# Performance work log

Measured on AMD Instinct MI355X. Metric: run time of the kernel, lower is better.

The kernel has to match this reference:

```python
import jax, jax.numpy as jnp
import numpy as np

N_NODES = 50000
IN_CH = 128
OUT_CH = 64
N_EDGES = 800000


def setup_inputs() -> dict:
    key = jax.random.key(0)
    k1, k2, k3, k4 = jax.random.split(key, 4)
    z = jax.random.normal(k1, (N_NODES, IN_CH), dtype=jnp.float32)
    edge_index = jax.random.randint(k2, (2, N_EDGES), 0, N_NODES, dtype=jnp.int64)
    # GCNConv params: weight [in, out] (glorot-ish), bias [out]
    W = jax.random.normal(k3, (IN_CH, OUT_CH), dtype=jnp.float32) / np.sqrt(IN_CH)
    b = jnp.zeros((OUT_CH,), dtype=jnp.float32)
    return {"z": z, "edge_index": edge_index, "W": W, "b": b}


def reference(z, edge_index, W, b):
    N = z.shape[0]
    # linear transform first (out_channels < in_channels reduces message traffic)
    x = z @ W  # [N, out]
    # add self-loops
    loop = jnp.arange(N, dtype=edge_index.dtype)
    src = jnp.concatenate([edge_index[0], loop])
    dst = jnp.concatenate([edge_index[1], loop])
    # symmetric normalization deg^-1/2 (degree counted on dst, incl. self-loops)
    deg = jnp.zeros((N,), dtype=x.dtype).at[dst].add(1.0)
    dinv = jnp.where(deg > 0, jax.lax.rsqrt(deg), 0.0)
    norm = dinv[src] * dinv[dst]  # [E+N]
    msg = x[src] * norm[:, None]  # gather + scale
    out = jax.ops.segment_sum(msg, dst, num_segments=N)  # scatter-add
    return jax.nn.relu(out + b)
```

## Files before the change

### kernel.cpp

```cpp
#include <hip/hip_runtime.h>

#define IN_CH 128
#define OUT_CH 64

#define CSHIFT 6
#define BNODES 64
#define NCMAX 1024
#define CAP 1536
#define BIN_EPT 8

typedef __attribute__((ext_vector_type(8))) short bf16x8;
typedef __attribute__((ext_vector_type(4))) float f32x4;

__device__ inline unsigned short f2bf(float x) {
    unsigned int u = __builtin_bit_cast(unsigned int, x);
    return (unsigned short)((u + 0x7FFFu + ((u >> 16) & 1u)) >> 16);
}
__device__ inline float bf2f(unsigned short h) {
    unsigned int u = ((unsigned int)h) << 16;
    return __builtin_bit_cast(float, u);
}

__global__ void bin_edges(const int* __restrict__ ei, int* __restrict__ gctr,
                          unsigned int* __restrict__ ebuf, int E, int NC) {
    __shared__ int cnt[NCMAX];
    __shared__ int gbase[NCMAX];
    for (int i = threadIdx.x; i < NC; i += blockDim.x) cnt[i] = 0;
    __syncthreads();

    unsigned int pk[BIN_EPT];
    int bk[BIN_EPT];
    int e0 = blockIdx.x * (blockDim.x * BIN_EPT) + threadIdx.x;
#pragma unroll
    for (int k = 0; k < BIN_EPT; ++k) {
        int e = e0 + k * blockDim.x;
        if (e < E) {
            int s = ei[e];
            int d = ei[E + e];
            pk[k] = ((unsigned int)d << 16) | (unsigned int)s;
            bk[k] = d >> CSHIFT;
            atomicAdd(&cnt[bk[k]], 1);
        } else bk[k] = -1;
    }
    __syncthreads();
    for (int i = threadIdx.x; i < NC; i += blockDim.x) {
        int c = cnt[i];
        gbase[i] = c ? atomicAdd(&gctr[i], c) : 0;
    }
    __syncthreads();
    for (int i = threadIdx.x; i < NC; i += blockDim.x) cnt[i] = 0;
    __syncthreads();
#pragma unroll
    for (int k = 0; k < BIN_EPT; ++k) {
        if (bk[k] >= 0) {
            int o = gbase[bk[k]] + atomicAdd(&cnt[bk[k]], 1);
            if (o < CAP)
                ebuf[(size_t)bk[k] * CAP + o] = pk[k];
        }
    }
}

__global__ void degree_dinv(const unsigned int* __restrict__ ebuf,
                            const int* __restrict__ gctr,
                            float* __restrict__ dinv, int N) {
    __shared__ int cnt[BNODES];
    const int b = blockIdx.x;
    const int n0 = b << CSHIFT;
    if (threadIdx.x < BNODES) cnt[threadIdx.x] = 0;
    __syncthreads();
    const int ecnt = min(gctr[b], CAP);
    const unsigned int* eb = ebuf + (size_t)b * CAP;
    for (int i = threadIdx.x; i < ecnt; i += blockDim.x)
        atomicAdd(&cnt[(int)(eb[i] >> 16) - n0], 1);
    __syncthreads();
    const int node = n0 + threadIdx.x;
    if (threadIdx.x < BNODES && node < N)
        dinv[node] = rsqrtf((float)(cnt[threadIdx.x] + 1));
}

__global__ void wfrag_prep(const float* __restrict__ W, unsigned short* __restrict__ wf) {
    for (int i = threadIdx.x; i < 4 * 4 * 64 * 8; i += blockDim.x) {
        int j    = i & 7;
        int lane = (i >> 3) & 63;
        int kk   = (i >> 9) & 3;
        int nt   = i >> 11;
        int k = kk * 32 + ((lane >> 4) & 3) * 8 + j;
        int n = nt * 16 + (lane & 15);
        wf[i] = f2bf(W[k * OUT_CH + n]);
    }
}

__global__ void gemm_mfma(const float* __restrict__ z,
                          const unsigned short* __restrict__ wfrag,
                          const float* __restrict__ dinv,
                          unsigned short* __restrict__ y, int N) {
    const int lane = threadIdx.x & 63;
    const int wid  = threadIdx.x >> 6;
    const int row0 = blockIdx.x * 64 + wid * 16;

    bf16x8 bfr[4][4];
#pragma unroll
    for (int nt = 0; nt < 4; ++nt)
#pragma unroll
        for (int kk = 0; kk < 4; ++kk)
            bfr[nt][kk] = *(const bf16x8*)&wfrag[(((nt * 4 + kk) * 64) + lane) * 8];

    f32x4 acc[4];
#pragma unroll
    for (int nt = 0; nt < 4; ++nt) acc[nt] = (f32x4){0.f, 0.f, 0.f, 0.f};

    const int arow = row0 + (lane & 15);
    const int zrow = (arow < N) ? arow : (N - 1);
    const int sub  = lane >> 4;
    const float* zr = z + (size_t)zrow * IN_CH + sub * 8;

#pragma unroll
    for (int kk = 0; kk < 4; ++kk) {
        float4 f0 = *(const float4*)(zr + kk * 32);
        float4 f1 = *(const float4*)(zr + kk * 32 + 4);
        bf16x8 a;
        a[0] = (short)f2bf(f0.x); a[1] = (short)f2bf(f0.y);
        a[2] = (short)f2bf(f0.z); a[3] = (short)f2bf(f0.w);
        a[4] = (short)f2bf(f1.x); a[5] = (short)f2bf(f1.y);
        a[6] = (short)f2bf(f1.z); a[7] = (short)f2bf(f1.w);
#pragma unroll
        for (int nt = 0; nt < 4; ++nt)
            acc[nt] = __builtin_amdgcn_mfma_f32_16x16x32_bf16(a, bfr[nt][kk], acc[nt], 0, 0, 0);
    }

    const int crow0 = row0 + sub * 4;
#pragma unroll
    for (int r = 0; r < 4; ++r) {
        int row = crow0 + r;
        if (row < N) {
            float di = dinv[row];
#pragma unroll
            for (int nt = 0; nt < 4; ++nt)
                y[(size_t)row * OUT_CH + nt * 16 + (lane & 15)] = f2bf(acc[nt][r] * di);
        }
    }
}

__global__ __launch_bounds__(512) void sort_gather(const unsigned int* __restrict__ ebuf,
                                                   const int* __restrict__ gctr,
                                                   const unsigned int* __restrict__ y2,
                                                   const float* __restrict__ dinv,
                                                   const float* __restrict__ bias,
                                                   float* __restrict__ out, int N) {
    __shared__ unsigned int epk[CAP];
    __shared__ unsigned short scol[CAP];
    __shared__ int cnt[BNODES];
    __shared__ int off[BNODES];
    const int b = blockIdx.x;
    const int n0 = b << CSHIFT;
    const int tid = threadIdx.x;
    const int ecnt = min(gctr[b], CAP);
    const unsigned int* eb = ebuf + (size_t)b * CAP;

    if (tid < BNODES) cnt[tid] = 0;
    __syncthreads();
    for (int i = tid; i < ecnt; i += 512) {
        unsigned int p = eb[i];
        epk[i] = p;
        atomicAdd(&cnt[(int)(p >> 16) - n0], 1);
    }
    __syncthreads();

    if (tid < BNODES) off[tid] = cnt[tid];
    __syncthreads();
    for (int o = 1; o < BNODES; o <<= 1) {
        int v = 0;
        if (tid < BNODES && tid >= o) v = off[tid - o];
        __syncthreads();
        if (tid < BNODES) off[tid] += v;
        __syncthreads();
    }
    if (tid < BNODES) { off[tid] -= cnt[tid]; cnt[tid] = off[tid]; }
    __syncthreads();

    for (int i = tid; i < ecnt; i += 512) {
        unsigned int p = epk[i];
        int rel = (int)(p >> 16) - n0;
        int slot = atomicAdd(&cnt[rel], 1);
        scol[slot] = (unsigned short)(p & 0xFFFFu);
    }
    __syncthreads();

    const int lane = tid & 63;
    const int w = tid >> 6;
    const int half = lane >> 5;
    const int c2 = lane & 31;
    const float2 bv = *(const float2*)&bias[c2 * 2];

#pragma unroll
    for (int rnd = 0; rnd < 4; ++rnd) {
        const int nrel = rnd * 16 + w * 2 + half;
        const int node = n0 + nrel;
        const bool valid = node < N;
        int j    = valid ? off[nrel] : 0;
        int cend = valid ? cnt[nrel] : 0;

        float accLo = 0.f, accHi = 0.f;
        if (valid) {
            unsigned int sv = y2[(size_t)node * 32 + c2];
            accLo = bf2f((unsigned short)(sv & 0xFFFFu));
            accHi = bf2f((unsigned short)(sv >> 16));
        }

        for (; j + 8 <= cend; j += 8) {
            int s0 = scol[j], s1 = scol[j+1], s2 = scol[j+2], s3 = scol[j+3];
            int s4 = scol[j+4], s5 = scol[j+5], s6 = scol[j+6], s7 = scol[j+7];
            unsigned int v0 = y2[(size_t)s0 * 32 + c2];
            unsigned int v1 = y2[(size_t)s1 * 32 + c2];
            unsigned int v2 = y2[(size_t)s2 * 32 + c2];
            unsigned int v3 = y2[(size_t)s3 * 32 + c2];
            unsigned int v4 = y2[(size_t)s4 * 32 + c2];
            unsigned int v5 = y2[(size_t)s5 * 32 + c2];
            unsigned int v6 = y2[(size_t)s6 * 32 + c2];
            unsigned int v7 = y2[(size_t)s7 * 32 + c2];
            accLo += bf2f((unsigned short)(v0 & 0xFFFFu)); accHi += bf2f((unsigned short)(v0 >> 16));
            accLo += bf2f((unsigned short)(v1 & 0xFFFFu)); accHi += bf2f((unsigned short)(v1 >> 16));
            accLo += bf2f((unsigned short)(v2 & 0xFFFFu)); accHi += bf2f((unsigned short)(v2 >> 16));
            accLo += bf2f((unsigned short)(v3 & 0xFFFFu)); accHi += bf2f((unsigned short)(v3 >> 16));
            accLo += bf2f((unsigned short)(v4 & 0xFFFFu)); accHi += bf2f((unsigned short)(v4 >> 16));
            accLo += bf2f((unsigned short)(v5 & 0xFFFFu)); accHi += bf2f((unsigned short)(v5 >> 16));
            accLo += bf2f((unsigned short)(v6 & 0xFFFFu)); accHi += bf2f((unsigned short)(v6 >> 16));
            accLo += bf2f((unsigned short)(v7 & 0xFFFFu)); accHi += bf2f((unsigned short)(v7 >> 16));
        }
        for (; j < cend; ++j) {
            unsigned int v = y2[(size_t)scol[j] * 32 + c2];
            accLo += bf2f((unsigned short)(v & 0xFFFFu));
            accHi += bf2f((unsigned short)(v >> 16));
        }

        if (valid) {
            float di = dinv[node];
            float2 o2;
            o2.x = fmaxf(fmaf(accLo, di, bv.x), 0.f);
            o2.y = fmaxf(fmaf(accHi, di, bv.y), 0.f);
            *(float2*)&out[(size_t)node * OUT_CH + c2 * 2] = o2;
        }
    }
}

extern "C" void kernel_launch(void* const* d_in, const int* in_sizes, int n_in,
                              void* d_out, int out_size, void* d_ws, size_t ws_size,
                              hipStream_t stream) {
    const float* z  = (const float*)d_in[0];
    const int*   ei = (const int*)d_in[1];
    const float* W  = (const float*)d_in[2];
    const float* b  = (const float*)d_in[3];
    float*       out = (float*)d_out;

    const int N = in_sizes[0] / IN_CH;
    const int E = in_sizes[1] / 2;
    const int NC = (N + BNODES - 1) >> CSHIFT;

    unsigned short* y     = (unsigned short*)d_ws;
    unsigned int*   ebuf  = (unsigned int*)(y + (size_t)N * OUT_CH);
    float*          dinv  = (float*)(ebuf + (size_t)NC * CAP);
    int*            gctr  = (int*)(dinv + N);
    unsigned short* wfrag = (unsigned short*)(((uintptr_t)(gctr + NC) + 15) & ~(uintptr_t)15);

    hipMemsetAsync(gctr, 0, (size_t)NC * sizeof(int), stream);

    const int binBlocks = (E + 256 * BIN_EPT - 1) / (256 * BIN_EPT);

    bin_edges  <<<binBlocks, 256, 0, stream>>>(ei, gctr, ebuf, E, NC);
    degree_dinv<<<NC, 256, 0, stream>>>(ebuf, gctr, dinv, N);
    wfrag_prep <<<1, 256, 0, stream>>>(W, wfrag);
    gemm_mfma  <<<(N + 63) / 64, 256, 0, stream>>>(z, wfrag, dinv, y, N);
    sort_gather<<<NC, 512, 0, stream>>>(ebuf, gctr, (const unsigned int*)y, dinv, b, out, N);
}
```

Before: 72.98 us.

## Vectorize edge loads, merge wfrag prep into degree kernel, mask gather tail

The binning kernel now gives each thread 8 contiguous edges and reads them with int4 vector loads instead of strided scalar loads. The W fragment preparation moves into an extra block of the degree kernel, removing one kernel launch. The gather loop handles the remainder with masked 8-wide batches so the tail also issues its loads in parallel, at the cost of some redundant loads. The edge-ordering change alters which bins get filled first, but counts are unchanged.

```diff
diff --git a/kernel.cpp b/kernel.cpp
--- a/kernel.cpp
+++ b/kernel.cpp
@@ -30,17 +30,33 @@
 
     unsigned int pk[BIN_EPT];
     int bk[BIN_EPT];
-    int e0 = blockIdx.x * (blockDim.x * BIN_EPT) + threadIdx.x;
-#pragma unroll
-    for (int k = 0; k < BIN_EPT; ++k) {
-        int e = e0 + k * blockDim.x;
-        if (e < E) {
-            int s = ei[e];
-            int d = ei[E + e];
-            pk[k] = ((unsigned int)d << 16) | (unsigned int)s;
-            bk[k] = d >> CSHIFT;
+    const int g0 = (blockIdx.x * blockDim.x + threadIdx.x) * BIN_EPT;
+
+    if (g0 + BIN_EPT <= E) {
+        int4 s0 = *(const int4*)(ei + g0);
+        int4 s1 = *(const int4*)(ei + g0 + 4);
+        int4 d0 = *(const int4*)(ei + E + g0);
+        int4 d1 = *(const int4*)(ei + E + g0 + 4);
+        int ss[BIN_EPT] = {s0.x, s0.y, s0.z, s0.w, s1.x, s1.y, s1.z, s1.w};
+        int dd[BIN_EPT] = {d0.x, d0.y, d0.z, d0.w, d1.x, d1.y, d1.z, d1.w};
+#pragma unroll
+        for (int k = 0; k < BIN_EPT; ++k) {
+            pk[k] = ((unsigned int)dd[k] << 16) | (unsigned int)ss[k];
+            bk[k] = dd[k] >> CSHIFT;
             atomicAdd(&cnt[bk[k]], 1);
-        } else bk[k] = -1;
+        }
+    } else {
+#pragma unroll
+        for (int k = 0; k < BIN_EPT; ++k) {
+            int e = g0 + k;
+            if (e < E) {
+                int s = ei[e];
+                int d = ei[E + e];
+                pk[k] = ((unsigned int)d << 16) | (unsigned int)s;
+                bk[k] = d >> CSHIFT;
+                atomicAdd(&cnt[bk[k]], 1);
+            } else bk[k] = -1;
+        }
     }
     __syncthreads();
     for (int i = threadIdx.x; i < NC; i += blockDim.x) {
@@ -60,11 +76,25 @@
     }
 }
 
-__global__ void degree_dinv(const unsigned int* __restrict__ ebuf,
-                            const int* __restrict__ gctr,
-                            float* __restrict__ dinv, int N) {
+__global__ void degree_wfrag(const unsigned int* __restrict__ ebuf,
+                             const int* __restrict__ gctr,
+                             float* __restrict__ dinv, int N, int NC,
+                             const float* __restrict__ W,
+                             unsigned short* __restrict__ wf) {
+    const int b = blockIdx.x;
+    if (b == NC) {
+        for (int i = threadIdx.x; i < 4 * 4 * 64 * 8; i += blockDim.x) {
+            int j    = i & 7;
+            int lane = (i >> 3) & 63;
+            int kk   = (i >> 9) & 3;
+            int nt   = i >> 11;
+            int k = kk * 32 + ((lane >> 4) & 3) * 8 + j;
+            int n = nt * 16 + (lane & 15);
+            wf[i] = f2bf(W[k * OUT_CH + n]);
+        }
+        return;
+    }
     __shared__ int cnt[BNODES];
-    const int b = blockIdx.x;
     const int n0 = b << CSHIFT;
     if (threadIdx.x < BNODES) cnt[threadIdx.x] = 0;
     __syncthreads();
@@ -76,18 +106,6 @@
     const int node = n0 + threadIdx.x;
     if (threadIdx.x < BNODES && node < N)
         dinv[node] = rsqrtf((float)(cnt[threadIdx.x] + 1));
-}
-
-__global__ void wfrag_prep(const float* __restrict__ W, unsigned short* __restrict__ wf) {
-    for (int i = threadIdx.x; i < 4 * 4 * 64 * 8; i += blockDim.x) {
-        int j    = i & 7;
-        int lane = (i >> 3) & 63;
-        int kk   = (i >> 9) & 3;
-        int nt   = i >> 11;
-        int k = kk * 32 + ((lane >> 4) & 3) * 8 + j;
-        int n = nt * 16 + (lane & 15);
-        wf[i] = f2bf(W[k * OUT_CH + n]);
-    }
 }
 
 __global__ void gemm_mfma(const float* __restrict__ z,
@@ -197,7 +215,7 @@
         const int nrel = rnd * 16 + w * 2 + half;
         const int node = n0 + nrel;
         const bool valid = node < N;
-        int j    = valid ? off[nrel] : 0;
+        int jbeg = valid ? off[nrel] : 0;
         int cend = valid ? cnt[nrel] : 0;
 
         float accLo = 0.f, accHi = 0.f;
@@ -207,30 +225,22 @@
             accHi = bf2f((unsigned short)(sv >> 16));
         }
 
-        for (; j + 8 <= cend; j += 8) {
-            int s0 = scol[j], s1 = scol[j+1], s2 = scol[j+2], s3 = scol[j+3];
-            int s4 = scol[j+4], s5 = scol[j+5], s6 = scol[j+6], s7 = scol[j+7];
-            unsigned int v0 = y2[(size_t)s0 * 32 + c2];
-            unsigned int v1 = y2[(size_t)s1 * 32 + c2];
-            unsigned int v2 = y2[(size_t)s2 * 32 + c2];
-            unsigned int v3 = y2[(size_t)s3 * 32 + c2];
-            unsigned int v4 = y2[(size_t)s4 * 32 + c2];
-            unsigned int v5 = y2[(size_t)s5 * 32 + c2];
-            unsigned int v6 = y2[(size_t)s6 * 32 + c2];
-            unsigned int v7 = y2[(size_t)s7 * 32 + c2];
-            accLo += bf2f((unsigned short)(v0 & 0xFFFFu)); accHi += bf2f((unsigned short)(v0 >> 16));
-            accLo += bf2f((unsigned short)(v1 & 0xFFFFu)); accHi += bf2f((unsigned short)(v1 >> 16));
-            accLo += bf2f((unsigned short)(v2 & 0xFFFFu)); accHi += bf2f((unsigned short)(v2 >> 16));
-            accLo += bf2f((unsigned short)(v3 & 0xFFFFu)); accHi += bf2f((unsigned short)(v3 >> 16));
-            accLo += bf2f((unsigned short)(v4 & 0xFFFFu)); accHi += bf2f((unsigned short)(v4 >> 16));
-            accLo += bf2f((unsigned short)(v5 & 0xFFFFu)); accHi += bf2f((unsigned short)(v5 >> 16));
-            accLo += bf2f((unsigned short)(v6 & 0xFFFFu)); accHi += bf2f((unsigned short)(v6 >> 16));
-            accLo += bf2f((unsigned short)(v7 & 0xFFFFu)); accHi += bf2f((unsigned short)(v7 >> 16));
-        }
-        for (; j < cend; ++j) {
-            unsigned int v = y2[(size_t)scol[j] * 32 + c2];
-            accLo += bf2f((unsigned short)(v & 0xFFFFu));
-            accHi += bf2f((unsigned short)(v >> 16));
+        for (int j = jbeg; j < cend; j += 8) {
+            unsigned int v[8]; bool m[8];
+#pragma unroll
+            for (int t = 0; t < 8; ++t) {
+                int jj = j + t;
+                m[t] = jj < cend;
+                int s = scol[m[t] ? jj : (cend - 1)];
+                v[t] = y2[(size_t)s * 32 + c2];
+            }
+#pragma unroll
+            for (int t = 0; t < 8; ++t) {
+                if (m[t]) {
+                    accLo += bf2f((unsigned short)(v[t] & 0xFFFFu));
+                    accHi += bf2f((unsigned short)(v[t] >> 16));
+                }
+            }
         }
 
         if (valid) {
@@ -266,9 +276,8 @@
 
     const int binBlocks = (E + 256 * BIN_EPT - 1) / (256 * BIN_EPT);
 
-    bin_edges  <<<binBlocks, 256, 0, stream>>>(ei, gctr, ebuf, E, NC);
-    degree_dinv<<<NC, 256, 0, stream>>>(ebuf, gctr, dinv, N);
-    wfrag_prep <<<1, 256, 0, stream>>>(W, wfrag);
-    gemm_mfma  <<<(N + 63) / 64, 256, 0, stream>>>(z, wfrag, dinv, y, N);
-    sort_gather<<<NC, 512, 0, stream>>>(ebuf, gctr, (const unsigned int*)y, dinv, b, out, N);
-}
+    bin_edges   <<<binBlocks, 256, 0, stream>>>(ei, gctr, ebuf, E, NC);
+    degree_wfrag<<<NC + 1, 256, 0, stream>>>(ebuf, gctr, dinv, N, NC, W, wfrag);
+    gemm_mfma   <<<(N + 63) / 64, 256, 0, stream>>>(z, wfrag, dinv, y, N);
+    sort_gather <<<NC, 512, 0, stream>>>(ebuf, gctr, (const unsigned int*)y, dinv, b, out, N);
+}
```

After: 72.09 us. About the same (-1.2%).
